# Kernel tuning notes

Hardware: AMD Instinct MI355X
Metric: run time of the kernel (lower is better)

The kernel has to match this reference:

```python
import jax, jax.numpy as jnp
import numpy as np
from jax import lax

K = 7          # attention window (attn_conv_props.kernel_size)
PAD = K // 2   # 'same' zero padding


def conv1x1(x, W, b):
    # x: (B, Cin, H, W), W: (Cout, Cin), b: (Cout,)
    return jnp.einsum('bchw,oc->bohw', x, W) + b[None, :, None, None]


def unfold(x, k=K):
    # torch Unfold with 'same' zero padding: (B, C, H, W) -> (B, C, k*k, H, W)
    # lax patches are channel-major over the C*k*k feature dim, matching torch.
    B, C, H, W = x.shape
    p = lax.conv_general_dilated_patches(
        x, filter_shape=(k, k), window_strides=(1, 1),
        padding=((PAD, PAD), (PAD, PAD)))
    return p.reshape(B, C, k * k, H, W)


def setup_inputs() -> dict:
    key = jax.random.key(0)
    ks = jax.random.split(key, 8)
    B, Cin, H, W = 2, 128, 64, 64
    heads, dk, dv, Cout = 8, 32, 32, 128
    s_in = 0.02
    return {
        'x':  jax.random.normal(ks[0], (B, Cin, H, W), jnp.float32),
        'Wk': jax.random.normal(ks[1], (heads * dk, Cin), jnp.float32) * s_in,
        'bk': jnp.zeros((heads * dk,), jnp.float32),
        'Wq': jax.random.normal(ks[2], (heads * dk, Cin), jnp.float32) * s_in,
        'bq': jnp.zeros((heads * dk,), jnp.float32),
        'Wv': jax.random.normal(ks[3], (heads * dv, Cin), jnp.float32) * s_in,
        'bv': jnp.zeros((heads * dv,), jnp.float32),
        'Wo': jax.random.normal(ks[4], (Cout, heads * dv), jnp.float32) * s_in,
        'bo': jnp.zeros((Cout,), jnp.float32),
    }


def reference(x, Wk, bk, Wq, bq, Wv, bv, Wo, bo):
    B, Cin, H, W = x.shape
    heads, dk = 8, 32
    dv = 32

    k = conv1x1(x, Wk, bk)   # (B, heads*dk, H, W)
    q = conv1x1(x, Wq, bq)   # (B, heads*dk, H, W)
    v = conv1x1(x, Wv, bv)   # (B, heads*dv, H, W)

    k_unf = unfold(k).reshape(B, heads, dk, K * K, H, W)  # (B,h,dk,A,H,W)
    v_unf = unfold(v).reshape(B, heads, dv, K * K, H, W)  # (B,h,dv,A,H,W)
    q_h = q.reshape(B, heads, dk, H, W)                   # (B,h,dk,H,W)

    scale = jnp.sqrt(jnp.asarray(dk, jnp.float32))
    # per-pixel window logits: (B, h, H, W, A)
    logits = jnp.einsum('bhdxy,bhdaxy->bhxya', q_h, k_unf) / scale
    score = jax.nn.softmax(logits, axis=-1)
    # attend over window: (B, h, dv, H, W)
    attn = jnp.einsum('bhxya,bhdaxy->bhdxy', score, v_unf)
    attn = attn.reshape(B, heads * dv, H, W)

    return conv1x1(attn, Wo, bo)  # (B, Cout, H, W)
```

## Files before the change

kernel.cpp:

```cpp
#include <hip/hip_runtime.h>
#include <hip/hip_bf16.h>
#include <math.h>

constexpr int HW = 4096;

using bf8   = __attribute__((ext_vector_type(8))) short;
using f32x4 = __attribute__((ext_vector_type(4))) float;

constexpr float SCALE = 0.17677669529663687f;


__global__ __launch_bounds__(256) void qkv_fused(
    const float* __restrict__ x,
    const float* __restrict__ Wk, const float* __restrict__ Wq,
    const float* __restrict__ Wv, const float* __restrict__ Wo,
    const float* __restrict__ bk, const float* __restrict__ bq,
    const float* __restrict__ bv,
    unsigned short* __restrict__ Qb, unsigned short* __restrict__ Kc,
    unsigned short* __restrict__ Vc, __hip_bfloat16* __restrict__ Wob)
{
    int bx = blockIdx.x, y = blockIdx.y;
    int t  = threadIdx.x;

    if (bx >= 128) {
        int bid2 = (bx - 128) * 12 + y;
        int base = bid2 * 256 + t;
        const int STR = 48 * 256;
        for (int i = base; i < 120832; i += STR) {
            int plane = i / 236;
            int c8    = i - plane * 236;
            int byteoff;
            if (c8 < 108) {
                int r6  = c8 / 18;
                int o8  = c8 - r6 * 18;
                int row = r6 < 3 ? r6 : 64 + r6;
                byteoff = row * 160 + o8 * 8;
            } else {
                int s   = c8 - 108;
                int row = 3 + (s >> 1);
                byteoff = row * 160 + ((s & 1) ? 136 : 0);
            }
            *(uint2*)((char*)Vc + (size_t)plane * 11200 + byteoff) = make_uint2(0u, 0u);
        }
        for (int i = base; i < 51456; i += STR) {
            int b   = i >= 25728;
            int r   = i - 25728 * b;
            int pxi = r >> 5;
            int sub = r & 31;
            int yy, xx;
            if (pxi < 420) {
                int r70 = pxi / 70;
                yy = r70 < 3 ? r70 : 64 + r70;
                xx = pxi - r70 * 70;
            } else {
                int q = pxi - 420;
                yy = q / 6 + 3;
                int c6 = q - (yy - 3) * 6;
                xx = c6 < 3 ? c6 : 64 + c6;
            }
            *(uint4*)&Kc[((size_t)b * 4900 + yy * 70 + xx) * 256 + sub * 8] =
                make_uint4(0u, 0u, 0u, 0u);
        }
        for (int i = base; i < 32768; i += STR)
            Wob[i] = __float2bfloat16(Wo[i]);
        return;
    }

    __shared__ __align__(16) unsigned short Xl[8192];
    __shared__ __align__(16) unsigned short Wl[8192];

    int b   = bx >> 6;
    int px0 = bx * 64;
    int hw0 = px0 & 4095;
    const float* Wm   = y < 4 ? Wk : (y < 8 ? Wq : Wv);
    const float* bias = y < 4 ? bk : (y < 8 ? bq : bv);
    int ocl = (y & 3) * 64;

    {
        int px = t >> 2;
        int q  = t & 3;
        int wv = px >> 4, mm = px & 15;
        const float* xp = x + ((size_t)b * 128 + q * 32) * HW + hw0 + px;
        int dbase = (wv * 4 + q) * 512 + mm * 8;
        #pragma unroll
        for (int kq = 0; kq < 4; ++kq) {
            union { __hip_bfloat16 hh[8]; uint4 u; } pk;
            #pragma unroll
            for (int j = 0; j < 8; ++j)
                pk.hh[j] = __float2bfloat16(xp[(size_t)(kq * 8 + j) * HW]);
            *(uint4*)&Xl[dbase + kq * 128] = pk.u;
        }
    }
    {
        int oc = t >> 2;
        int q  = t & 3;
        int of = oc >> 4, mm = oc & 15;
        const float* wp = Wm + (size_t)(ocl + oc) * 128 + q * 32;
        int dbase = (of * 4 + q) * 512 + mm * 8;
        #pragma unroll
        for (int kq = 0; kq < 4; ++kq) {
            float4 a0 = *(const float4*)(wp + kq * 8);
            float4 a1 = *(const float4*)(wp + kq * 8 + 4);
            union { __hip_bfloat16 hh[8]; uint4 u; } pk;
            pk.hh[0] = __float2bfloat16(a0.x); pk.hh[1] = __float2bfloat16(a0.y);
            pk.hh[2] = __float2bfloat16(a0.z); pk.hh[3] = __float2bfloat16(a0.w);
            pk.hh[4] = __float2bfloat16(a1.x); pk.hh[5] = __float2bfloat16(a1.y);
            pk.hh[6] = __float2bfloat16(a1.z); pk.hh[7] = __float2bfloat16(a1.w);
            *(uint4*)&Wl[dbase + kq * 128] = pk.u;
        }
    }
    __syncthreads();

    int w = t >> 6, lane = t & 63;
    int m  = lane & 15;
    int kq = lane >> 4;
    int pxw = px0 + w * 16;

    bf8 aF[4];
    #pragma unroll
    for (int ks = 0; ks < 4; ++ks)
        aF[ks] = *(const bf8*)&Xl[(w * 4 + ks) * 512 + lane * 8];

    f32x4 acc[4] = { {0.f,0.f,0.f,0.f}, {0.f,0.f,0.f,0.f},
                     {0.f,0.f,0.f,0.f}, {0.f,0.f,0.f,0.f} };
    #pragma unroll
    for (int ks = 0; ks < 4; ++ks) {
        #pragma unroll
        for (int of = 0; of < 4; ++of) {
            bf8 bF = *(const bf8*)&Wl[(of * 4 + ks) * 512 + lane * 8];
            acc[of] = __builtin_amdgcn_mfma_f32_16x16x32_bf16(aF[ks], bF, acc[of], 0, 0, 0);
        }
    }

    if (y >= 4 && y < 8) {
        #pragma unroll
        for (int of = 0; of < 4; ++of) {
            float bval = bias[ocl + of * 16 + m];
            #pragma unroll
            for (int r = 0; r < 4; ++r) {
                int px = pxw + kq * 4 + r;
                float v = (acc[of][r] + bval) * SCALE;
                __hip_bfloat16 hv = __float2bfloat16(v);
                unsigned us = *(unsigned short*)&hv;
                unsigned un = __shfl_xor((int)us, 1);
                if (!(m & 1))
                    *(unsigned*)&Qb[(size_t)px * 256 + ocl + of * 16 + m] = us | (un << 16);
            }
        }
    } else if (y < 4) {
        #pragma unroll
        for (int of = 0; of < 4; ++of) {
            float bval = bias[ocl + of * 16 + m];
            #pragma unroll
            for (int r = 0; r < 4; ++r) {
                int px = pxw + kq * 4 + r;
                int bb = px >> 12, hw = px & 4095;
                int yy = hw >> 6, xx = hw & 63;
                __hip_bfloat16 hv = __float2bfloat16(acc[of][r] + bval);
                unsigned us = *(unsigned short*)&hv;
                unsigned un = __shfl_xor((int)us, 1);
                if (!(m & 1))
                    *(unsigned*)&Kc[((size_t)bb * 4900 + (yy + 3) * 70 + xx + 3) * 256
                                    + ocl + of * 16 + m] = us | (un << 16);
            }
        }
    } else {
        #pragma unroll
        for (int of = 0; of < 4; ++of) {
            float bval = bias[ocl + of * 16 + m];
            int ch = ocl + of * 16 + m;
            union { __hip_bfloat16 h[4]; uint2 u; } pk;
            #pragma unroll
            for (int r = 0; r < 4; ++r)
                pk.h[r] = __float2bfloat16(acc[of][r] + bval);
            int px = pxw + kq * 4;
            int bb = px >> 12, hw = px & 4095;
            int yy = hw >> 6, xx = hw & 63;
            *(uint2*)&Vc[((size_t)bb * 256 + ch) * 5600 + (yy + 3) * 80 + xx + 4] = pk.u;
        }
    }
}

__global__ __launch_bounds__(512, 4) void attn_proj(
    const unsigned short* __restrict__ Qb, const unsigned short* __restrict__ Kc,
    const unsigned short* __restrict__ Vc, const __hip_bfloat16* __restrict__ Wob,
    const float* __restrict__ bo, float* __restrict__ out)
{
    __shared__ __align__(16) unsigned short P[8 * 2176];
    __shared__ __align__(16) unsigned short AB[16 * 264];

    int id   = blockIdx.x;
    int b    = id >> 8;
    int tile = id & 255;
    int ty0  = (tile >> 3) * 2;
    int tx0  = (tile & 7) * 8;

    int t  = threadIdx.x;
    int w  = t >> 6;
    int l  = t & 63;
    int lr = l & 15;
    int g  = l >> 4;
    int h  = w;

    unsigned short* pw = &P[w * 2176];
    const unsigned short* kcb = Kc + (size_t)b * (4900 * 256) + h * 32 + g * 8;

    int apy = lr >> 3;
    int apx = lr & 7;
    bf8 aQ = *(const bf8*)(Qb +
        ((size_t)b * 4096 + (ty0 + apy) * 64 + tx0 + apx) * 256 + h * 32 + g * 8);

    f32x4 acc[8];
    #pragma unroll
    for (int i = 0; i < 8; ++i) {
        bf8 bK = *(const bf8*)(kcb + ((size_t)(ty0 + i) * 70 + tx0 + lr - 1) * 256);
        f32x4 z = {0.f, 0.f, 0.f, 0.f};
        acc[i] = __builtin_amdgcn_mfma_f32_16x16x32_bf16(aQ, bK, z, 0, 0, 0);
    }

    int gy2 = g >> 1;
    float rsum[4] = {0.f, 0.f, 0.f, 0.f};
    #pragma unroll
    for (int i = 0; i < 8; ++i) {
        bool dyok = ((unsigned)(i - gy2)) <= 6u;
        #pragma unroll
        for (int reg = 0; reg < 4; ++reg) {
            int px_ = ((g & 1) << 2) + reg;
            bool ok = dyok && (((unsigned)(lr - px_ - 1)) <= 6u);
            float e = ok ? __expf(acc[i][reg]) : 0.f;
            rsum[reg] += e;
            __hip_bfloat16 hb = __float2bfloat16(e);
            unsigned us = *(unsigned short*)&hb;
            unsigned un = __shfl_xor((int)us, 1);
            if (!(l & 1))
                *(unsigned*)&pw[(g * 4 + reg) * 136 + i * 16 + lr] = us | (un << 16);
        }
    }
    #pragma unroll
    for (int reg = 0; reg < 4; ++reg) {
        float sm = rsum[reg];
        sm += __shfl_xor(sm, 1);
        sm += __shfl_xor(sm, 2);
        sm += __shfl_xor(sm, 4);
        sm += __shfl_xor(sm, 8);
        rsum[reg] = 1.f / sm;
    }

    f32x4 pv[2] = { {0.f,0.f,0.f,0.f}, {0.f,0.f,0.f,0.f} };
    #pragma unroll
    for (int ks = 0; ks < 4; ++ks) {
        bf8 aP = *(const bf8*)&pw[lr * 136 + ks * 32 + g * 8];
        int yq = 2 * ks + (g >> 1);
        int xv = (g & 1) << 3;
        #pragma unroll
        for (int nt2 = 0; nt2 < 2; ++nt2) {
            bf8 bV = *(const bf8*)(Vc +
                ((size_t)b * 256 + h * 32 + nt2 * 16 + lr) * 5600 +
                (ty0 + yq) * 80 + tx0 + xv);
            pv[nt2] = __builtin_amdgcn_mfma_f32_16x16x32_bf16(aP, bV, pv[nt2], 0, 0, 0);
        }
    }

    #pragma unroll
    for (int nt2 = 0; nt2 < 2; ++nt2) {
        #pragma unroll
        for (int reg = 0; reg < 4; ++reg) {
            float ov = pv[nt2][reg] * rsum[reg];
            __hip_bfloat16 hb = __float2bfloat16(ov);
            unsigned us = *(unsigned short*)&hb;
            unsigned un = __shfl_xor((int)us, 1);
            if (!(l & 1)) {
                int rloc = g * 4 + reg;
                *(unsigned*)&AB[rloc * 264 + h * 32 + nt2 * 16 + lr] = us | (un << 16);
            }
        }
    }
    __syncthreads();

    f32x4 po = {0.f, 0.f, 0.f, 0.f};
    #pragma unroll
    for (int ks = 0; ks < 8; ++ks) {
        bf8 aA = *(const bf8*)&AB[lr * 264 + ks * 32 + g * 8];
        bf8 bF = *(const bf8*)((const unsigned short*)Wob +
                 (size_t)(w * 16 + lr) * 256 + ks * 32 + g * 8);
        po = __builtin_amdgcn_mfma_f32_16x16x32_bf16(aA, bF, po, 0, 0, 0);
    }
    {
        int oc = w * 16 + lr;
        float bval = bo[oc];
        int q_  = g * 4;
        int py  = q_ >> 3;
        int px_ = q_ & 7;
        float4 r4 = make_float4(po[0] + bval, po[1] + bval,
                                po[2] + bval, po[3] + bval);
        *(float4*)&out[((size_t)b * 128 + oc) * 4096 + (ty0 + py) * 64 + tx0 + px_] = r4;
    }
}

extern "C" void kernel_launch(void* const* d_in, const int* in_sizes, int n_in,
                              void* d_out, int out_size, void* d_ws, size_t ws_size,
                              hipStream_t stream) {
    const float* x  = (const float*)d_in[0];
    const float* Wk = (const float*)d_in[1];
    const float* bk = (const float*)d_in[2];
    const float* Wq = (const float*)d_in[3];
    const float* bq = (const float*)d_in[4];
    const float* Wv = (const float*)d_in[5];
    const float* bv = (const float*)d_in[6];
    const float* Wo = (const float*)d_in[7];
    const float* bo = (const float*)d_in[8];
    float* out = (float*)d_out;

    char* wsb = (char*)d_ws;
    unsigned short* Qb  = (unsigned short*)wsb;
    unsigned short* Kc  = (unsigned short*)(wsb + (4u << 20));
    unsigned short* Vc  = (unsigned short*)(wsb + (9u << 20));
    __hip_bfloat16* Wob = (__hip_bfloat16*)(wsb + (15u << 20));

    qkv_fused<<<dim3(132, 12), 256, 0, stream>>>(
        x, Wk, Wq, Wv, Wo, bk, bq, bv, Qb, Kc, Vc, Wob);
    attn_proj<<<dim3(512), 512, 0, stream>>>(Qb, Kc, Vc, Wob, bo, out);
}
```

Before: 42.13 us.

## Fuse QKV projection into attention kernel with per-tile halo recompute in LDS

Replaces the two-kernel pipeline with a single kernel. Each tile loads an x halo into LDS, computes Q, K and V for that halo with MFMA, then runs windowed attention and the output projection. This removes the global workspace writes and reads of Q, K, V and the second launch. In exchange, K and V are recomputed redundantly across neighbouring tiles, fp32 weights are converted per block, and the large LDS footprint limits occupancy to one block per CU.

```diff
diff --git a/kernel.cpp b/kernel.cpp
--- a/kernel.cpp
+++ b/kernel.cpp
@@ -9,189 +9,34 @@
 
 constexpr float SCALE = 0.17677669529663687f;
 
-
-__global__ __launch_bounds__(256) void qkv_fused(
+__device__ __forceinline__ bf8 ldW8(const float* p) {
+    float4 a0 = *(const float4*)p;
+    float4 a1 = *(const float4*)(p + 4);
+    union { __hip_bfloat16 hh[8]; bf8 v; } pk;
+    pk.hh[0] = __float2bfloat16(a0.x); pk.hh[1] = __float2bfloat16(a0.y);
+    pk.hh[2] = __float2bfloat16(a0.z); pk.hh[3] = __float2bfloat16(a0.w);
+    pk.hh[4] = __float2bfloat16(a1.x); pk.hh[5] = __float2bfloat16(a1.y);
+    pk.hh[6] = __float2bfloat16(a1.z); pk.hh[7] = __float2bfloat16(a1.w);
+    return pk.v;
+}
+
+__global__ __launch_bounds__(512) void fused_one(
     const float* __restrict__ x,
     const float* __restrict__ Wk, const float* __restrict__ Wq,
     const float* __restrict__ Wv, const float* __restrict__ Wo,
     const float* __restrict__ bk, const float* __restrict__ bq,
-    const float* __restrict__ bv,
-    unsigned short* __restrict__ Qb, unsigned short* __restrict__ Kc,
-    unsigned short* __restrict__ Vc, __hip_bfloat16* __restrict__ Wob)
+    const float* __restrict__ bv, const float* __restrict__ bo,
+    float* __restrict__ out)
 {
-    int bx = blockIdx.x, y = blockIdx.y;
-    int t  = threadIdx.x;
-
-    if (bx >= 128) {
-        int bid2 = (bx - 128) * 12 + y;
-        int base = bid2 * 256 + t;
-        const int STR = 48 * 256;
-        for (int i = base; i < 120832; i += STR) {
-            int plane = i / 236;
-            int c8    = i - plane * 236;
-            int byteoff;
-            if (c8 < 108) {
-                int r6  = c8 / 18;
-                int o8  = c8 - r6 * 18;
-                int row = r6 < 3 ? r6 : 64 + r6;
-                byteoff = row * 160 + o8 * 8;
-            } else {
-                int s   = c8 - 108;
-                int row = 3 + (s >> 1);
-                byteoff = row * 160 + ((s & 1) ? 136 : 0);
-            }
-            *(uint2*)((char*)Vc + (size_t)plane * 11200 + byteoff) = make_uint2(0u, 0u);
-        }
-        for (int i = base; i < 51456; i += STR) {
-            int b   = i >= 25728;
-            int r   = i - 25728 * b;
-            int pxi = r >> 5;
-            int sub = r & 31;
-            int yy, xx;
-            if (pxi < 420) {
-                int r70 = pxi / 70;
-                yy = r70 < 3 ? r70 : 64 + r70;
-                xx = pxi - r70 * 70;
-            } else {
-                int q = pxi - 420;
-                yy = q / 6 + 3;
-                int c6 = q - (yy - 3) * 6;
-                xx = c6 < 3 ? c6 : 64 + c6;
-            }
-            *(uint4*)&Kc[((size_t)b * 4900 + yy * 70 + xx) * 256 + sub * 8] =
-                make_uint4(0u, 0u, 0u, 0u);
-        }
-        for (int i = base; i < 32768; i += STR)
-            Wob[i] = __float2bfloat16(Wo[i]);
-        return;
-    }
-
-    __shared__ __align__(16) unsigned short Xl[8192];
-    __shared__ __align__(16) unsigned short Wl[8192];
-
-    int b   = bx >> 6;
-    int px0 = bx * 64;
-    int hw0 = px0 & 4095;
-    const float* Wm   = y < 4 ? Wk : (y < 8 ? Wq : Wv);
-    const float* bias = y < 4 ? bk : (y < 8 ? bq : bv);
-    int ocl = (y & 3) * 64;
-
-    {
-        int px = t >> 2;
-        int q  = t & 3;
-        int wv = px >> 4, mm = px & 15;
-        const float* xp = x + ((size_t)b * 128 + q * 32) * HW + hw0 + px;
-        int dbase = (wv * 4 + q) * 512 + mm * 8;
-        #pragma unroll
-        for (int kq = 0; kq < 4; ++kq) {
-            union { __hip_bfloat16 hh[8]; uint4 u; } pk;
-            #pragma unroll
-            for (int j = 0; j < 8; ++j)
-                pk.hh[j] = __float2bfloat16(xp[(size_t)(kq * 8 + j) * HW]);
-            *(uint4*)&Xl[dbase + kq * 128] = pk.u;
-        }
-    }
-    {
-        int oc = t >> 2;
-        int q  = t & 3;
-        int of = oc >> 4, mm = oc & 15;
-        const float* wp = Wm + (size_t)(ocl + oc) * 128 + q * 32;
-        int dbase = (of * 4 + q) * 512 + mm * 8;
-        #pragma unroll
-        for (int kq = 0; kq < 4; ++kq) {
-            float4 a0 = *(const float4*)(wp + kq * 8);
-            float4 a1 = *(const float4*)(wp + kq * 8 + 4);
-            union { __hip_bfloat16 hh[8]; uint4 u; } pk;
-            pk.hh[0] = __float2bfloat16(a0.x); pk.hh[1] = __float2bfloat16(a0.y);
-            pk.hh[2] = __float2bfloat16(a0.z); pk.hh[3] = __float2bfloat16(a0.w);
-            pk.hh[4] = __float2bfloat16(a1.x); pk.hh[5] = __float2bfloat16(a1.y);
-            pk.hh[6] = __float2bfloat16(a1.z); pk.hh[7] = __float2bfloat16(a1.w);
-            *(uint4*)&Wl[dbase + kq * 128] = pk.u;
-        }
-    }
-    __syncthreads();
-
-    int w = t >> 6, lane = t & 63;
-    int m  = lane & 15;
-    int kq = lane >> 4;
-    int pxw = px0 + w * 16;
-
-    bf8 aF[4];
-    #pragma unroll
-    for (int ks = 0; ks < 4; ++ks)
-        aF[ks] = *(const bf8*)&Xl[(w * 4 + ks) * 512 + lane * 8];
-
-    f32x4 acc[4] = { {0.f,0.f,0.f,0.f}, {0.f,0.f,0.f,0.f},
-                     {0.f,0.f,0.f,0.f}, {0.f,0.f,0.f,0.f} };
-    #pragma unroll
-    for (int ks = 0; ks < 4; ++ks) {
-        #pragma unroll
-        for (int of = 0; of < 4; ++of) {
-            bf8 bF = *(const bf8*)&Wl[(of * 4 + ks) * 512 + lane * 8];
-            acc[of] = __builtin_amdgcn_mfma_f32_16x16x32_bf16(aF[ks], bF, acc[of], 0, 0, 0);
-        }
-    }
-
-    if (y >= 4 && y < 8) {
-        #pragma unroll
-        for (int of = 0; of < 4; ++of) {
-            float bval = bias[ocl + of * 16 + m];
-            #pragma unroll
-            for (int r = 0; r < 4; ++r) {
-                int px = pxw + kq * 4 + r;
-                float v = (acc[of][r] + bval) * SCALE;
-                __hip_bfloat16 hv = __float2bfloat16(v);
-                unsigned us = *(unsigned short*)&hv;
-                unsigned un = __shfl_xor((int)us, 1);
-                if (!(m & 1))
-                    *(unsigned*)&Qb[(size_t)px * 256 + ocl + of * 16 + m] = us | (un << 16);
-            }
-        }
-    } else if (y < 4) {
-        #pragma unroll
-        for (int of = 0; of < 4; ++of) {
-            float bval = bias[ocl + of * 16 + m];
-            #pragma unroll
-            for (int r = 0; r < 4; ++r) {
-                int px = pxw + kq * 4 + r;
-                int bb = px >> 12, hw = px & 4095;
-                int yy = hw >> 6, xx = hw & 63;
-                __hip_bfloat16 hv = __float2bfloat16(acc[of][r] + bval);
-                unsigned us = *(unsigned short*)&hv;
-                unsigned un = __shfl_xor((int)us, 1);
-                if (!(m & 1))
-                    *(unsigned*)&Kc[((size_t)bb * 4900 + (yy + 3) * 70 + xx + 3) * 256
-                                    + ocl + of * 16 + m] = us | (un << 16);
-            }
-        }
-    } else {
-        #pragma unroll
-        for (int of = 0; of < 4; ++of) {
-            float bval = bias[ocl + of * 16 + m];
-            int ch = ocl + of * 16 + m;
-            union { __hip_bfloat16 h[4]; uint2 u; } pk;
-            #pragma unroll
-            for (int r = 0; r < 4; ++r)
-                pk.h[r] = __float2bfloat16(acc[of][r] + bval);
-            int px = pxw + kq * 4;
-            int bb = px >> 12, hw = px & 4095;
-            int yy = hw >> 6, xx = hw & 63;
-            *(uint2*)&Vc[((size_t)bb * 256 + ch) * 5600 + (yy + 3) * 80 + xx + 4] = pk.u;
-        }
-    }
-}
-
-__global__ __launch_bounds__(512, 4) void attn_proj(
-    const unsigned short* __restrict__ Qb, const unsigned short* __restrict__ Kc,
-    const unsigned short* __restrict__ Vc, const __hip_bfloat16* __restrict__ Wob,
-    const float* __restrict__ bo, float* __restrict__ out)
-{
-    __shared__ __align__(16) unsigned short P[8 * 2176];
-    __shared__ __align__(16) unsigned short AB[16 * 264];
-
-    int id   = blockIdx.x;
-    int b    = id >> 8;
-    int tile = id & 255;
+    extern __shared__ __align__(16) unsigned short LDS[];
+    unsigned short* XT = LDS;
+    unsigned short* KT = LDS + 17408;
+    unsigned short* QT = LDS + 52224;
+    unsigned short* P  = LDS + 56448;
+
+    int bid  = blockIdx.x;
+    int b    = bid >> 8;
+    int tile = bid & 255;
     int ty0  = (tile >> 3) * 2;
     int tx0  = (tile & 7) * 8;
 
@@ -202,90 +47,211 @@
     int g  = l >> 4;
     int h  = w;
 
+    {
+        int hcol = t & 15;
+        int hrow = (t >> 4) & 7;
+        int cq   = t >> 7;
+        int ir = ty0 + hrow - 3; ir = ir < 0 ? 0 : (ir > 63 ? 63 : ir);
+        int ic = tx0 + hcol - 4; ic = ic < 0 ? 0 : (ic > 63 ? 63 : ic);
+        const float* xp = x + ((size_t)b * 128 + cq * 32) * HW + ir * 64 + ic;
+        int hb = (hrow * 16 + hcol) * 136 + cq * 32;
+        #pragma unroll
+        for (int i = 0; i < 32; i += 2) {
+            __hip_bfloat16 h0 = __float2bfloat16(xp[(size_t)i * HW]);
+            __hip_bfloat16 h1 = __float2bfloat16(xp[(size_t)(i + 1) * HW]);
+            unsigned u = (unsigned)*(unsigned short*)&h0 |
+                         ((unsigned)*(unsigned short*)&h1 << 16);
+            *(unsigned*)&XT[hb + i] = u;
+        }
+    }
+    __syncthreads();
+
+    {
+        int hpQ = ((lr >> 3) + 3) * 16 + (lr & 7) + 4;
+        #pragma unroll
+        for (int oi = 0; oi < 2; ++oi) {
+            int ot = w * 2 + oi;
+            f32x4 acc = {0.f, 0.f, 0.f, 0.f};
+            #pragma unroll
+            for (int ks = 0; ks < 4; ++ks) {
+                bf8 aX = *(const bf8*)&XT[hpQ * 136 + ks * 32 + g * 8];
+                bf8 bW = ldW8(Wq + (size_t)(ot * 16 + lr) * 128 + ks * 32 + g * 8);
+                acc = __builtin_amdgcn_mfma_f32_16x16x32_bf16(aX, bW, acc, 0, 0, 0);
+            }
+            float bval = bq[ot * 16 + lr];
+            #pragma unroll
+            for (int r = 0; r < 4; ++r) {
+                float v = (acc[r] + bval) * SCALE;
+                __hip_bfloat16 hv = __float2bfloat16(v);
+                unsigned us = *(unsigned short*)&hv;
+                unsigned un = __shfl_xor((int)us, 1);
+                if (!(l & 1))
+                    *(unsigned*)&QT[(g * 4 + r) * 264 + ot * 16 + lr] = us | (un << 16);
+            }
+        }
+        bf8 bW[2][4];
+        float bvalK[2];
+        #pragma unroll
+        for (int oi = 0; oi < 2; ++oi) {
+            int ot = w * 2 + oi;
+            #pragma unroll
+            for (int ks = 0; ks < 4; ++ks)
+                bW[oi][ks] = ldW8(Wk + (size_t)(ot * 16 + lr) * 128 + ks * 32 + g * 8);
+            bvalK[oi] = bk[ot * 16 + lr];
+        }
+        #pragma unroll
+        for (int pt = 0; pt < 8; ++pt) {
+            bf8 aX[4];
+            #pragma unroll
+            for (int ks = 0; ks < 4; ++ks)
+                aX[ks] = *(const bf8*)&XT[(pt * 16 + lr) * 136 + ks * 32 + g * 8];
+            int ir = ty0 + pt - 3;
+            bool rok = (ir >= 0) && (ir < 64);
+            #pragma unroll
+            for (int oi = 0; oi < 2; ++oi) {
+                f32x4 acc = {0.f, 0.f, 0.f, 0.f};
+                #pragma unroll
+                for (int ks = 0; ks < 4; ++ks)
+                    acc = __builtin_amdgcn_mfma_f32_16x16x32_bf16(aX[ks], bW[oi][ks], acc, 0, 0, 0);
+                int ot = w * 2 + oi;
+                #pragma unroll
+                for (int r = 0; r < 4; ++r) {
+                    int ic = tx0 + g * 4 + r - 4;
+                    bool ok = rok && (ic >= 0) && (ic < 64);
+                    float v = ok ? (acc[r] + bvalK[oi]) : 0.f;
+                    __hip_bfloat16 hv = __float2bfloat16(v);
+                    unsigned us = *(unsigned short*)&hv;
+                    unsigned un = __shfl_xor((int)us, 1);
+                    if (!(l & 1))
+                        *(unsigned*)&KT[(pt * 16 + g * 4 + r) * 264 + ot * 16 + lr] =
+                            us | (un << 16);
+                }
+            }
+        }
+    }
+    __syncthreads();
+
     unsigned short* pw = &P[w * 2176];
-    const unsigned short* kcb = Kc + (size_t)b * (4900 * 256) + h * 32 + g * 8;
-
-    int apy = lr >> 3;
-    int apx = lr & 7;
-    bf8 aQ = *(const bf8*)(Qb +
-        ((size_t)b * 4096 + (ty0 + apy) * 64 + tx0 + apx) * 256 + h * 32 + g * 8);
-
-    f32x4 acc[8];
-    #pragma unroll
-    for (int i = 0; i < 8; ++i) {
-        bf8 bK = *(const bf8*)(kcb + ((size_t)(ty0 + i) * 70 + tx0 + lr - 1) * 256);
-        f32x4 z = {0.f, 0.f, 0.f, 0.f};
-        acc[i] = __builtin_amdgcn_mfma_f32_16x16x32_bf16(aQ, bK, z, 0, 0, 0);
-    }
-
-    int gy2 = g >> 1;
-    float rsum[4] = {0.f, 0.f, 0.f, 0.f};
-    #pragma unroll
-    for (int i = 0; i < 8; ++i) {
-        bool dyok = ((unsigned)(i - gy2)) <= 6u;
+    float rsum[4];
+    {
+        bf8 aQ = *(const bf8*)&QT[lr * 264 + h * 32 + g * 8];
+        f32x4 acc8[8];
+        #pragma unroll
+        for (int i = 0; i < 8; ++i) {
+            bf8 bK = *(const bf8*)&KT[(i * 16 + lr) * 264 + h * 32 + g * 8];
+            f32x4 z = {0.f, 0.f, 0.f, 0.f};
+            acc8[i] = __builtin_amdgcn_mfma_f32_16x16x32_bf16(aQ, bK, z, 0, 0, 0);
+        }
+        int gy2 = g >> 1;
+        rsum[0] = rsum[1] = rsum[2] = rsum[3] = 0.f;
+        #pragma unroll
+        for (int i = 0; i < 8; ++i) {
+            bool dyok = ((unsigned)(i - gy2)) <= 6u;
+            #pragma unroll
+            for (int reg = 0; reg < 4; ++reg) {
+                int px_ = ((g & 1) << 2) + reg;
+                bool ok = dyok && (((unsigned)(lr - px_ - 1)) <= 6u);
+                float e = ok ? __expf(acc8[i][reg]) : 0.f;
+                rsum[reg] += e;
+                __hip_bfloat16 hb = __float2bfloat16(e);
+                unsigned us = *(unsigned short*)&hb;
+                unsigned un = __shfl_xor((int)us, 1);
+                if (!(l & 1))
+                    *(unsigned*)&pw[(g * 4 + reg) * 136 + i * 16 + lr] = us | (un << 16);
+            }
+        }
         #pragma unroll
         for (int reg = 0; reg < 4; ++reg) {
-            int px_ = ((g & 1) << 2) + reg;
-            bool ok = dyok && (((unsigned)(lr - px_ - 1)) <= 6u);
-            float e = ok ? __expf(acc[i][reg]) : 0.f;
-            rsum[reg] += e;
-            __hip_bfloat16 hb = __float2bfloat16(e);
-            unsigned us = *(unsigned short*)&hb;
-            unsigned un = __shfl_xor((int)us, 1);
-            if (!(l & 1))
-                *(unsigned*)&pw[(g * 4 + reg) * 136 + i * 16 + lr] = us | (un << 16);
-        }
-    }
-    #pragma unroll
-    for (int reg = 0; reg < 4; ++reg) {
-        float sm = rsum[reg];
-        sm += __shfl_xor(sm, 1);
-        sm += __shfl_xor(sm, 2);
-        sm += __shfl_xor(sm, 4);
-        sm += __shfl_xor(sm, 8);
-        rsum[reg] = 1.f / sm;
-    }
-
-    f32x4 pv[2] = { {0.f,0.f,0.f,0.f}, {0.f,0.f,0.f,0.f} };
-    #pragma unroll
-    for (int ks = 0; ks < 4; ++ks) {
-        bf8 aP = *(const bf8*)&pw[lr * 136 + ks * 32 + g * 8];
-        int yq = 2 * ks + (g >> 1);
-        int xv = (g & 1) << 3;
+            float sm = rsum[reg];
+            sm += __shfl_xor(sm, 1);
+            sm += __shfl_xor(sm, 2);
+            sm += __shfl_xor(sm, 4);
+            sm += __shfl_xor(sm, 8);
+            rsum[reg] = 1.f / sm;
+        }
+    }
+    __syncthreads();
+
+    unsigned short* VT = KT;
+    {
+        bf8 bW[2][4];
+        float bvalV[2];
+        #pragma unroll
+        for (int oi = 0; oi < 2; ++oi) {
+            int ot = w * 2 + oi;
+            #pragma unroll
+            for (int ks = 0; ks < 4; ++ks)
+                bW[oi][ks] = ldW8(Wv + (size_t)(ot * 16 + lr) * 128 + ks * 32 + g * 8);
+            bvalV[oi] = bv[ot * 16 + lr];
+        }
+        #pragma unroll
+        for (int pt = 0; pt < 8; ++pt) {
+            bf8 aX[4];
+            #pragma unroll
+            for (int ks = 0; ks < 4; ++ks)
+                aX[ks] = *(const bf8*)&XT[(pt * 16 + lr) * 136 + ks * 32 + g * 8];
+            int ir = ty0 + pt - 3;
+            bool rok = (ir >= 0) && (ir < 64);
+            #pragma unroll
+            for (int oi = 0; oi < 2; ++oi) {
+                f32x4 acc = {0.f, 0.f, 0.f, 0.f};
+                #pragma unroll
+                for (int ks = 0; ks < 4; ++ks)
+                    acc = __builtin_amdgcn_mfma_f32_16x16x32_bf16(aX[ks], bW[oi][ks], acc, 0, 0, 0);
+                int ot = w * 2 + oi;
+                union { __hip_bfloat16 h4[4]; uint2 u; } pk;
+                #pragma unroll
+                for (int r = 0; r < 4; ++r) {
+                    int ic = tx0 + g * 4 + r - 4;
+                    bool ok = rok && (ic >= 0) && (ic < 64);
+                    pk.h4[r] = __float2bfloat16(ok ? (acc[r] + bvalV[oi]) : 0.f);
+                }
+                *(uint2*)&VT[(size_t)(ot * 16 + lr) * 136 + pt * 16 + g * 4] = pk.u;
+            }
+        }
+    }
+    __syncthreads();
+
+    unsigned short* AB = QT;
+    {
+        f32x4 pv[2] = { {0.f,0.f,0.f,0.f}, {0.f,0.f,0.f,0.f} };
+        #pragma unroll
+        for (int ks = 0; ks < 4; ++ks) {
+            bf8 aP = *(const bf8*)&pw[lr * 136 + ks * 32 + g * 8];
+            int yq = 2 * ks + (g >> 1);
+            int xv = (g & 1) << 3;
+            #pragma unroll
+            for (int nt2 = 0; nt2 < 2; ++nt2) {
+                bf8 bV = *(const bf8*)&VT[(size_t)(h * 32 + nt2 * 16 + lr) * 136 +
+                                          yq * 16 + xv];
+                pv[nt2] = __builtin_amdgcn_mfma_f32_16x16x32_bf16(aP, bV, pv[nt2], 0, 0, 0);
+            }
+        }
         #pragma unroll
         for (int nt2 = 0; nt2 < 2; ++nt2) {
-            bf8 bV = *(const bf8*)(Vc +
-                ((size_t)b * 256 + h * 32 + nt2 * 16 + lr) * 5600 +
-                (ty0 + yq) * 80 + tx0 + xv);
-            pv[nt2] = __builtin_amdgcn_mfma_f32_16x16x32_bf16(aP, bV, pv[nt2], 0, 0, 0);
-        }
-    }
-
-    #pragma unroll
-    for (int nt2 = 0; nt2 < 2; ++nt2) {
-        #pragma unroll
-        for (int reg = 0; reg < 4; ++reg) {
-            float ov = pv[nt2][reg] * rsum[reg];
-            __hip_bfloat16 hb = __float2bfloat16(ov);
-            unsigned us = *(unsigned short*)&hb;
-            unsigned un = __shfl_xor((int)us, 1);
-            if (!(l & 1)) {
-                int rloc = g * 4 + reg;
-                *(unsigned*)&AB[rloc * 264 + h * 32 + nt2 * 16 + lr] = us | (un << 16);
-            }
-        }
-    }
-    __syncthreads();
-
-    f32x4 po = {0.f, 0.f, 0.f, 0.f};
-    #pragma unroll
-    for (int ks = 0; ks < 8; ++ks) {
-        bf8 aA = *(const bf8*)&AB[lr * 264 + ks * 32 + g * 8];
-        bf8 bF = *(const bf8*)((const unsigned short*)Wob +
-                 (size_t)(w * 16 + lr) * 256 + ks * 32 + g * 8);
-        po = __builtin_amdgcn_mfma_f32_16x16x32_bf16(aA, bF, po, 0, 0, 0);
-    }
-    {
+            #pragma unroll
+            for (int reg = 0; reg < 4; ++reg) {
+                float ov = pv[nt2][reg] * rsum[reg];
+                __hip_bfloat16 hb = __float2bfloat16(ov);
+                unsigned us = *(unsigned short*)&hb;
+                unsigned un = __shfl_xor((int)us, 1);
+                if (!(l & 1)) {
+                    int rloc = g * 4 + reg;
+                    *(unsigned*)&AB[rloc * 264 + h * 32 + nt2 * 16 + lr] = us | (un << 16);
+                }
+            }
+        }
+    }
+    __syncthreads();
+
+    {
+        f32x4 po = {0.f, 0.f, 0.f, 0.f};
+        #pragma unroll
+        for (int ks = 0; ks < 8; ++ks) {
+            bf8 aA  = *(const bf8*)&AB[lr * 264 + ks * 32 + g * 8];
+            bf8 bWo = ldW8(Wo + (size_t)(w * 16 + lr) * 256 + ks * 32 + g * 8);
+            po = __builtin_amdgcn_mfma_f32_16x16x32_bf16(aA, bWo, po, 0, 0, 0);
+        }
         int oc = w * 16 + lr;
         float bval = bo[oc];
         int q_  = g * 4;
@@ -311,13 +277,9 @@
     const float* bo = (const float*)d_in[8];
     float* out = (float*)d_out;
 
-    char* wsb = (char*)d_ws;
-    unsigned short* Qb  = (unsigned short*)wsb;
-    unsigned short* Kc  = (unsigned short*)(wsb + (4u << 20));
-    unsigned short* Vc  = (unsigned short*)(wsb + (9u << 20));
-    __hip_bfloat16* Wob = (__hip_bfloat16*)(wsb + (15u << 20));
-
-    qkv_fused<<<dim3(132, 12), 256, 0, stream>>>(
-        x, Wk, Wq, Wv, Wo, bk, bq, bv, Qb, Kc, Vc, Wob);
-    attn_proj<<<dim3(512), 512, 0, stream>>>(Qb, Kc, Vc, Wob, bo, out);
+    constexpr int LDS_BYTES = 147712;
+    hipFuncSetAttribute((const void*)fused_one,
+                        hipFuncAttributeMaxDynamicSharedMemorySize, LDS_BYTES);
+    fused_one<<<dim3(512), dim3(512), LDS_BYTES, stream>>>(
+        x, Wk, Wq, Wv, Wo, bk, bq, bv, bo, out);
 }
```

New measurement: 60.26 us. +43.0%, slower.
